# Performance work log

Hardware: AMD Instinct MI355X
Metric: run time of the kernel (lower is better)

The kernel has to match this reference:

```python
import jax, jax.numpy as jnp
import numpy as np

L, B, D, H, P = 4096, 4, 1024, 16, 256
HD = D // H
EPS = 1e-5


def _layer_norm(x, g, b):
    m = jnp.mean(x, axis=-1, keepdims=True)
    v = jnp.mean(jnp.square(x - m), axis=-1, keepdims=True)
    return (x - m) / jnp.sqrt(v + EPS) * g + b


def setup_inputs() -> dict:
    key = jax.random.key(0)
    ks = jax.random.split(key, 8)
    w = lambda k, shape: jax.random.normal(k, shape, jnp.float32) * 0.02
    return {
        "query": jax.random.normal(ks[0], (L, B, D), jnp.float32),
        "q_w": w(ks[1], (D, D)), "q_b": jnp.zeros((D,), jnp.float32),
        "k_w": w(ks[2], (D, D)), "k_b": jnp.zeros((D,), jnp.float32),
        "v_w": w(ks[3], (D, D)), "v_b": jnp.zeros((D,), jnp.float32),
        "e_weight": w(ks[4], (1, H, P, HD)),
        "e_out_w": w(ks[5], (D, D)), "e_out_b": jnp.zeros((D,), jnp.float32),
        "ln_g": jnp.ones((D,), jnp.float32), "ln_b": jnp.zeros((D,), jnp.float32),
        "out_w": w(ks[6], (D, D)), "out_b": jnp.zeros((D,), jnp.float32),
    }


def reference(query, q_w, q_b, k_w, k_b, v_w, v_b, e_weight,
              e_out_w, e_out_b, ln_g, ln_b, out_w, out_b):
    scaling = HD ** -0.5
    # ---- _compute_kv (kv_same=True, no padding mask) ----
    # kv: (L,B,D) -> (B,H,HD,L)
    kvh = query.reshape(L, B, H, HD).transpose(1, 2, 3, 0)
    # pkv = relu(E @ (kv * scaling)) : (B,H,P,L)
    pkv = jax.nn.relu(jnp.einsum('hpd,bhdl->bhpl', e_weight[0], kvh * scaling))
    # kv = pkv @ kv^T : (B,H,P,HD)
    kv = jnp.einsum('bhpl,bhdl->bhpd', pkv, kvh)
    # -> (P,B,D), e_out linear, residual add of e_weight, layer norm
    kv = kv.transpose(2, 0, 1, 3).reshape(P, B, D)
    kv = kv @ e_out_w.T + e_out_b
    kv = kv.reshape(P, B, H, HD) + e_weight.transpose(2, 0, 1, 3)  # broadcast (P,1,H,HD)
    kv = _layer_norm(kv.reshape(P, B, D), ln_g, ln_b)  # (P,B,D)

    # ---- standard MHA against the compressed kv ----
    q = (query @ q_w.T + q_b) * scaling            # (L,B,D)
    k = kv @ k_w.T + k_b                           # (P,B,D)
    v = kv @ v_w.T + v_b                           # (P,B,D)
    qh = q.reshape(L, B, H, HD)
    kh = k.reshape(P, B, H, HD)
    vh = v.reshape(P, B, H, HD)
    logits = jnp.einsum('lbhd,pbhd->bhlp', qh, kh)
    probs = jax.nn.softmax(logits, axis=-1)
    attn = jnp.einsum('bhlp,pbhd->lbhd', probs, vh).reshape(L, B, D)
    return attn @ out_w.T + out_b
```

## Files before the change

### kernel.cpp

```cpp
#include <hip/hip_runtime.h>
#include <hip/hip_bf16.h>
#include <cstdint>
#include <cstddef>

#define LL 4096
#define BB 4
#define DD 1024
#define HH 16
#define PP 256
#define HDD 64
#define LC 16
#define LCHUNK 256

constexpr float kScaling = 0.125f;
constexpr float kEps = 1e-5f;

typedef __attribute__((ext_vector_type(8))) short bf16x8;
typedef __attribute__((ext_vector_type(4))) short short4v;
typedef __attribute__((ext_vector_type(4))) float f32x4;

#define MFMA16(a, b, c) __builtin_amdgcn_mfma_f32_16x16x32_bf16((a), (b), (c), 0, 0, 0)

__device__ __forceinline__ unsigned short f2bf(float f) {
  unsigned int u = __builtin_bit_cast(unsigned int, f);
  u += 0x7FFFu + ((u >> 16) & 1u);
  return (unsigned short)(u >> 16);
}
__device__ __forceinline__ float bf2f(unsigned short u) {
  return __builtin_bit_cast(float, ((unsigned int)u) << 16);
}

__device__ __forceinline__ void gll16(const void* g, void* l) {
  __builtin_amdgcn_global_load_lds(
      (const __attribute__((address_space(1))) unsigned int*)g,
      (__attribute__((address_space(3))) unsigned int*)l, 16, 0, 0);
}

__global__ __launch_bounds__(256) void k_cvt_all(
    const float* __restrict__ q,
    const float* __restrict__ w0, const float* __restrict__ w1,
    const float* __restrict__ w2, const float* __restrict__ w3,
    const float* __restrict__ w4, const float* __restrict__ w5,
    unsigned short* __restrict__ dq,
    unsigned short* __restrict__ d0, unsigned short* __restrict__ d1,
    unsigned short* __restrict__ d2, unsigned short* __restrict__ d3,
    unsigned short* __restrict__ d4, unsigned short* __restrict__ d5) {
  int i = blockIdx.x * 256 + threadIdx.x;
  const float* src; unsigned short* dst; int off;
  if (i < 2097152) { src = q; dst = dq; off = i; }
  else {
    int j = i - 2097152; int w = j >> 17; off = j & 131071;
    if (w == 0) { src = w0; dst = d0; }
    else if (w == 1) { src = w1; dst = d1; }
    else if (w == 2) { src = w2; dst = d2; }
    else if (w == 3) { src = w3; dst = d3; }
    else if (w == 4) { src = w4; dst = d4; }
    else { if (off >= 32768) return; src = w5; dst = d5; }
  }
  const float4* s = (const float4*)(src + (size_t)off * 8);
  float4 a = s[0], b = s[1];
  bf16x8 o;
  o[0] = f2bf(a.x); o[1] = f2bf(a.y); o[2] = f2bf(a.z); o[3] = f2bf(a.w);
  o[4] = f2bf(b.x); o[5] = f2bf(b.y); o[6] = f2bf(b.z); o[7] = f2bf(b.w);
  *(bf16x8*)(dst + (size_t)off * 8) = o;
}

__global__ __launch_bounds__(256) void k_compress_mfma(
    const unsigned short* __restrict__ qbf, const unsigned short* __restrict__ ewbf,
    unsigned short* __restrict__ parts) {
  const int bh = blockIdx.x, lc = blockIdx.y;
  const int b = bh >> 4, h = bh & 15;
  const int tid = threadIdx.x, wv = tid >> 6, lane = tid & 63;
  const int fr = lane & 15, fg = lane >> 4;

  __shared__ __align__(16) char Xl[8192];
  __shared__ __align__(16) char Xtl[8192];
  __shared__ __align__(16) char Pl[32768];

  bf16x8 ef[4][2];
#pragma unroll
  for (int pt = 0; pt < 4; ++pt)
#pragma unroll
    for (int kc = 0; kc < 2; ++kc)
      ef[pt][kc] = *(const bf16x8*)(ewbf +
          (size_t)((h * PP + wv * 64 + pt * 16 + fr) * HDD) + kc * 32 + fg * 8);

  f32x4 acc[4][4];
#pragma unroll
  for (int i = 0; i < 4; ++i)
#pragma unroll
    for (int j = 0; j < 4; ++j) acc[i][j] = (f32x4){0.f, 0.f, 0.f, 0.f};

  const int l0 = lc * LCHUNK;
  for (int t = 0; t < 4; ++t) {
    __syncthreads();
    {
      int l2 = tid >> 3, c8 = tid & 7;
      int l = 2 * l2;
      const unsigned short* xp = qbf +
          ((size_t)(l0 + t * 64 + l) * BB + b) * DD + h * HDD + c8 * 8;
      bf16x8 v0 = *(const bf16x8*)xp;
      bf16x8 v1 = *(const bf16x8*)(xp + BB * DD);
      *(bf16x8*)(Xl + l * 128 + ((c8 ^ (l & 7)) << 4)) = v0;
      *(bf16x8*)(Xl + (l + 1) * 128 + ((c8 ^ ((l + 1) & 7)) << 4)) = v1;
#pragma unroll
      for (int i = 0; i < 8; ++i) {
        int dd = c8 * 8 + i;
        unsigned int packed = (unsigned int)(unsigned short)v0[i] |
                              ((unsigned int)(unsigned short)v1[i] << 16);
        *(unsigned int*)(Xtl + dd * 128 +
            ((((l >> 3) ^ (dd & 7) ^ (dd >> 3)) & 7) << 4) + ((l & 7) << 1)) = packed;
      }
    }
    __syncthreads();
#pragma unroll
    for (int lt = 0; lt < 4; ++lt) {
      int rl = lt * 16 + fr;
      bf16x8 xa0 = *(const bf16x8*)(Xl + rl * 128 + (((0 + fg) ^ (rl & 7)) << 4));
      bf16x8 xa1 = *(const bf16x8*)(Xl + rl * 128 + (((4 + fg) ^ (rl & 7)) << 4));
#pragma unroll
      for (int pt = 0; pt < 4; ++pt) {
        f32x4 s = (f32x4){0.f, 0.f, 0.f, 0.f};
        s = MFMA16(xa0, ef[pt][0], s);
        s = MFMA16(xa1, ef[pt][1], s);
        short4v pk;
#pragma unroll
        for (int r = 0; r < 4; ++r)
          pk[r] = (short)f2bf(fmaxf(s[r] * kScaling, 0.f));
        int p = wv * 64 + pt * 16 + fr;
        int lbase = lt * 16 + fg * 4;
        int slot = lbase >> 3;
        *(short4v*)(Pl + p * 128 + ((slot ^ (p & 7)) << 4) + ((lbase & 7) << 1)) = pk;
      }
    }
    asm volatile("s_waitcnt lgkmcnt(0)" ::: "memory");
    __builtin_amdgcn_sched_barrier(0);
#pragma unroll
    for (int kc = 0; kc < 2; ++kc) {
      bf16x8 pa[4], xb[4];
#pragma unroll
      for (int pt = 0; pt < 4; ++pt) {
        int p = wv * 64 + pt * 16 + fr;
        pa[pt] = *(const bf16x8*)(Pl + p * 128 + (((kc * 4 + fg) ^ (p & 7)) << 4));
      }
#pragma unroll
      for (int dt = 0; dt < 4; ++dt) {
        int dd = dt * 16 + fr;
        xb[dt] = *(const bf16x8*)(Xtl + dd * 128 +
                  ((((kc * 4 + fg) ^ (dd & 7) ^ (dd >> 3)) & 7) << 4));
      }
#pragma unroll
      for (int pt = 0; pt < 4; ++pt)
#pragma unroll
        for (int dt = 0; dt < 4; ++dt)
          acc[pt][dt] = MFMA16(pa[pt], xb[dt], acc[pt][dt]);
    }
  }
  unsigned short* op = parts + (size_t)(lc * 64 + bh) * PP * HDD;
#pragma unroll
  for (int pt = 0; pt < 4; ++pt)
#pragma unroll
    for (int dt = 0; dt < 4; ++dt)
#pragma unroll
      for (int r = 0; r < 4; ++r) {
        int p = wv * 64 + pt * 16 + fg * 4 + r;
        int dd = dt * 16 + fr;
        op[(size_t)p * HDD + dd] = f2bf(acc[pt][dt][r]);
      }
}

__global__ __launch_bounds__(256) void k_reduce(const unsigned short* __restrict__ parts,
                                                unsigned short* __restrict__ kv_raw_bf) {
  int i = blockIdx.x * 256 + threadIdx.x;
  float s = 0.f;
#pragma unroll
  for (int lcc = 0; lcc < LC; ++lcc) s += bf2f(parts[(size_t)lcc * (64 * PP * HDD) + i]);
  int d = i & 63, p = (i >> 6) & 255, bh = i >> 14;
  int b = bh >> 4, h = bh & 15;
  kv_raw_bf[(size_t)(p * BB + b) * DD + h * HDD + d] = f2bf(s);
}

template <int MODE, typename OUTT>
__device__ __forceinline__ void gemm_body(
    const unsigned short* __restrict__ A, const unsigned short* __restrict__ W,
    const float* __restrict__ bias, const float* __restrict__ ew,
    OUTT* __restrict__ C, int m0, int n0, char* Al, char* Bl) {
  const int tid = threadIdx.x;
  const int wv = tid >> 6, lane = tid & 63;
  const int fr = lane & 15, fg = lane >> 4;
  const int wr = wv >> 1, wc = wv & 1;

  f32x4 acc[4][4];
#pragma unroll
  for (int i = 0; i < 4; ++i)
#pragma unroll
    for (int j = 0; j < 4; ++j) acc[i][j] = (f32x4){0.f, 0.f, 0.f, 0.f};

  for (int k0 = 0; k0 < DD; k0 += 64) {
    __syncthreads();
#pragma unroll
    for (int j = 0; j < 4; ++j) {
      int u = tid + j * 256;
      int row = u >> 3, slot = u & 7;
      size_t gcol = (size_t)(k0 + 8 * (slot ^ (row & 7)));
      gll16(A + (size_t)(m0 + row) * DD + gcol, Al + u * 16);
      gll16(W + (size_t)(n0 + row) * DD + gcol, Bl + u * 16);
    }
    __syncthreads();
#pragma unroll
    for (int kc = 0; kc < 2; ++kc) {
      bf16x8 af[4], bfr[4];
#pragma unroll
      for (int mt = 0; mt < 4; ++mt) {
        int r = wr * 64 + mt * 16 + fr;
        af[mt] = *(const bf16x8*)(Al + r * 128 + (((kc * 4 + fg) ^ (r & 7)) << 4));
      }
#pragma unroll
      for (int nt = 0; nt < 4; ++nt) {
        int r = wc * 64 + nt * 16 + fr;
        bfr[nt] = *(const bf16x8*)(Bl + r * 128 + (((kc * 4 + fg) ^ (r & 7)) << 4));
      }
#pragma unroll
      for (int mt = 0; mt < 4; ++mt)
#pragma unroll
        for (int nt = 0; nt < 4; ++nt)
          acc[mt][nt] = MFMA16(af[mt], bfr[nt], acc[mt][nt]);
    }
  }

  float bs[4];
#pragma unroll
  for (int nt = 0; nt < 4; ++nt) bs[nt] = bias[n0 + wc * 64 + nt * 16 + fr];
#pragma unroll
  for (int mt = 0; mt < 4; ++mt)
#pragma unroll
    for (int nt = 0; nt < 4; ++nt) {
      int n = n0 + wc * 64 + nt * 16 + fr;
#pragma unroll
      for (int r = 0; r < 4; ++r) {
        int m = m0 + wr * 64 + mt * 16 + fg * 4 + r;
        float v = acc[mt][nt][r] + bs[nt];
        if (MODE == 1) v *= kScaling;
        if (MODE == 2) {
          int p = m >> 2, hh = n >> 6, d2 = n & 63;
          v += ew[(size_t)((hh << 8) + p) * HDD + d2];
        }
        if constexpr (sizeof(OUTT) == 2)
          C[(size_t)m * DD + n] = (OUTT)f2bf(v);
        else
          C[(size_t)m * DD + n] = v;
      }
    }
}

template <int MODE, typename OUTT>
__global__ __launch_bounds__(256) void k_gemm_mfma(
    const unsigned short* __restrict__ A, const unsigned short* __restrict__ W,
    const float* __restrict__ bias, const float* __restrict__ ew,
    OUTT* __restrict__ C) {
  __shared__ __align__(16) char Al[16384];
  __shared__ __align__(16) char Bl[16384];
  gemm_body<MODE, OUTT>(A, W, bias, ew, C, blockIdx.x * 128, blockIdx.y * 128, Al, Bl);
}

__global__ __launch_bounds__(256) void k_gemm_kv(
    const unsigned short* __restrict__ A,
    const unsigned short* __restrict__ Wk, const unsigned short* __restrict__ Wv,
    const float* __restrict__ kb, const float* __restrict__ vb,
    unsigned short* __restrict__ Ck, unsigned short* __restrict__ Cv) {
  __shared__ __align__(16) char Al[16384];
  __shared__ __align__(16) char Bl[16384];
  if (blockIdx.z == 0)
    gemm_body<0, unsigned short>(A, Wk, kb, nullptr, Ck,
                                 blockIdx.x * 128, blockIdx.y * 128, Al, Bl);
  else
    gemm_body<0, unsigned short>(A, Wv, vb, nullptr, Cv,
                                 blockIdx.x * 128, blockIdx.y * 128, Al, Bl);
}

template <int MODE, typename OUTT>
__global__ __launch_bounds__(512, 2) void k_gemm256(
    const unsigned short* __restrict__ A, const unsigned short* __restrict__ W,
    const float* __restrict__ bias, OUTT* __restrict__ C) {
  __shared__ __align__(16) char lds[131072];
  const int tid = threadIdx.x;
  const int wv = tid >> 6, lane = tid & 63;
  const int fr = lane & 15, fg = lane >> 4;
  const int wm = wv >> 2, wn = wv & 3;
  const int m0 = blockIdx.x * 256, n0 = blockIdx.y * 256;
  const int srow = tid >> 2, sslot = tid & 3;

  auto stageHalf = [&](const unsigned short* __restrict__ G, int g0, int colbase,
                       int dstBase) {
#pragma unroll
    for (int j = 0; j < 2; ++j) {
      int row = srow + j * 128;
      int gs = sslot ^ ((row >> 1) & 3);
      gll16(G + (size_t)(g0 + row) * DD + colbase + gs * 8,
            lds + dstBase + (tid + j * 512) * 16);
    }
  };
  auto rdA = [&](int mf, int kc, int cb) -> bf16x8 {
    int r = wm * 128 + mf * 16 + fr;
    return *(const bf16x8*)(lds + cb + kc * 16384 + r * 64 +
                            ((fg ^ ((r >> 1) & 3)) << 4));
  };
  auto rdB = [&](int nf, int kc, int cb) -> bf16x8 {
    int r = wn * 64 + nf * 16 + fr;
    return *(const bf16x8*)(lds + cb + 32768 + kc * 16384 + r * 64 +
                            ((fg ^ ((r >> 1) & 3)) << 4));
  };

  f32x4 acc[8][4];
#pragma unroll
  for (int i = 0; i < 8; ++i)
#pragma unroll
    for (int j = 0; j < 4; ++j) acc[i][j] = (f32x4){0.f, 0.f, 0.f, 0.f};
  bf16x8 a[8], b[4];

  stageHalf(A, m0, 0, 0);
  stageHalf(W, n0, 0, 32768);
  stageHalf(A, m0, 32, 16384);
  stageHalf(W, n0, 32, 32768 + 16384);
  stageHalf(A, m0, 64, 65536);
  stageHalf(W, n0, 64, 65536 + 32768);
  asm volatile("s_waitcnt vmcnt(4)" ::: "memory");
  __builtin_amdgcn_s_barrier();

  const int NT = DD / 64;
  for (int t = 0; t < NT; ++t) {
    const int cb = (t & 1) << 16;
    const int nb = cb ^ 65536;
    const int k1 = (t + 1) * 64, k2 = (t + 2) * 64;

#pragma unroll
    for (int i = 0; i < 8; ++i) a[i] = rdA(i, 0, cb);
#pragma unroll
    for (int i = 0; i < 4; ++i) b[i] = rdB(i, 0, cb);
    if (t + 1 < NT) {
      stageHalf(A, m0, k1 + 32, nb + 16384);
      stageHalf(W, n0, k1 + 32, nb + 32768 + 16384);
    }
    asm volatile("s_waitcnt lgkmcnt(0)" ::: "memory");
    __builtin_amdgcn_sched_barrier(0);
    __builtin_amdgcn_s_setprio(1);
#pragma unroll
    for (int mf = 0; mf < 8; ++mf)
#pragma unroll
      for (int nf = 0; nf < 4; ++nf)
        acc[mf][nf] = MFMA16(a[mf], b[nf], acc[mf][nf]);
    __builtin_amdgcn_s_setprio(0);
    __builtin_amdgcn_s_barrier();

#pragma unroll
    for (int i = 0; i < 8; ++i) a[i] = rdA(i, 1, cb);
#pragma unroll
    for (int i = 0; i < 4; ++i) b[i] = rdB(i, 1, cb);
    if (t + 2 < NT) {
      stageHalf(A, m0, k2, cb);
      stageHalf(W, n0, k2, cb + 32768);
    }
    asm volatile("s_waitcnt lgkmcnt(0)" ::: "memory");
    __builtin_amdgcn_sched_barrier(0);
    __builtin_amdgcn_s_setprio(1);
#pragma unroll
    for (int mf = 0; mf < 8; ++mf)
#pragma unroll
      for (int nf = 0; nf < 4; ++nf)
        acc[mf][nf] = MFMA16(a[mf], b[nf], acc[mf][nf]);
    __builtin_amdgcn_s_setprio(0);
    if (t + 2 < NT) {
      asm volatile("s_waitcnt vmcnt(4)" ::: "memory");
    } else if (t + 1 < NT) {
      asm volatile("s_waitcnt vmcnt(0)" ::: "memory");
    }
    __builtin_amdgcn_s_barrier();
  }

  float bs[4];
#pragma unroll
  for (int nf = 0; nf < 4; ++nf) bs[nf] = bias[n0 + wn * 64 + nf * 16 + fr];
#pragma unroll
  for (int mf = 0; mf < 8; ++mf)
#pragma unroll
    for (int nf = 0; nf < 4; ++nf) {
      int n = n0 + wn * 64 + nf * 16 + fr;
#pragma unroll
      for (int r = 0; r < 4; ++r) {
        int m = m0 + wm * 128 + mf * 16 + fg * 4 + r;
        float v = acc[mf][nf][r] + bs[nf];
        if (MODE == 1) v *= kScaling;
        if constexpr (sizeof(OUTT) == 2)
          C[(size_t)m * DD + n] = (OUTT)f2bf(v);
        else
          C[(size_t)m * DD + n] = v;
      }
    }
}

__global__ __launch_bounds__(256) void k_ln(const float* __restrict__ x,
                                            const float* __restrict__ g,
                                            const float* __restrict__ bb,
                                            unsigned short* __restrict__ y) {
  const int r = blockIdx.x;
  const int tid = threadIdx.x;
  const float* xr = x + (size_t)r * DD;
  float4 v = *(const float4*)(xr + tid * 4);
  float s1 = v.x + v.y + v.z + v.w;
  float s2 = v.x * v.x + v.y * v.y + v.z * v.z + v.w * v.w;
#pragma unroll
  for (int off = 32; off > 0; off >>= 1) {
    s1 += __shfl_down(s1, off);
    s2 += __shfl_down(s2, off);
  }
  __shared__ float w1[4], w2[4];
  if ((tid & 63) == 0) { w1[tid >> 6] = s1; w2[tid >> 6] = s2; }
  __syncthreads();
  float S1 = w1[0] + w1[1] + w1[2] + w1[3];
  float S2 = w2[0] + w2[1] + w2[2] + w2[3];
  float mean = S1 * (1.f / DD);
  float var = S2 * (1.f / DD) - mean * mean;
  float rstd = rsqrtf(var + kEps);
  float4 gv = *(const float4*)(g + tid * 4);
  float4 bv = *(const float4*)(bb + tid * 4);
  short4v o;
  o[0] = (short)f2bf((v.x - mean) * rstd * gv.x + bv.x);
  o[1] = (short)f2bf((v.y - mean) * rstd * gv.y + bv.y);
  o[2] = (short)f2bf((v.z - mean) * rstd * gv.z + bv.z);
  o[3] = (short)f2bf((v.w - mean) * rstd * gv.w + bv.w);
  *(short4v*)(y + (size_t)r * DD + tid * 4) = o;
}

__global__ __launch_bounds__(512, 2) void k_attn_mfma(
    const unsigned short* __restrict__ qbf, const unsigned short* __restrict__ kbf,
    const unsigned short* __restrict__ vbf, unsigned short* __restrict__ attn) {
  const int bh = blockIdx.y;
  const int b = bh >> 4, h = bh & 15;
  const int tid = threadIdx.x, wv = tid >> 6, lane = tid & 63;
  const int fr = lane & 15, fg = lane >> 4;
  const int bl0 = blockIdx.x * 128;

  __shared__ __align__(16) char Kl[16384];
  __shared__ __align__(16) char Vt[16384];
  __shared__ __align__(16) char Pl[32768];

  const size_t qrow = ((size_t)(bl0 + wv * 16 + fr) * BB + b) * DD + h * HDD;
  bf16x8 qf0 = *(const bf16x8*)(qbf + qrow + fg * 8);
  bf16x8 qf1 = *(const bf16x8*)(qbf + qrow + 32 + fg * 8);

  f32x4 o[4];
#pragma unroll
  for (int dt = 0; dt < 4; ++dt) o[dt] = (f32x4){0.f, 0.f, 0.f, 0.f};
  float psum = 0.f;
  char* Pw = Pl + wv * 4096;

  for (int ph = 0; ph < 2; ++ph) {
    __syncthreads();
#pragma unroll
    for (int j = 0; j < 2; ++j) {
      int u = tid + j * 512;
      int p = u >> 3, slot = u & 7;
      gll16(kbf + ((size_t)((ph * 128 + p) * BB + b)) * DD + h * HDD +
                8 * (slot ^ (p & 7)),
            Kl + u * 16);
    }
    {
      int p2 = tid >> 3, c8 = tid & 7;
      int p0 = ph * 128 + 2 * p2;
      const unsigned short* vp = vbf + ((size_t)(p0 * BB + b)) * DD + h * HDD + c8 * 8;
      bf16x8 v0 = *(const bf16x8*)vp;
      bf16x8 v1 = *(const bf16x8*)(vp + BB * DD);
      int pl = (2 * p2) & 63, pc = p2 >> 5;
      char* base = Vt + pc * 8192;
#pragma unroll
      for (int i = 0; i < 8; ++i) {
        int dd = c8 * 8 + i;
        unsigned int packed = (unsigned int)(unsigned short)v0[i] |
                              ((unsigned int)(unsigned short)v1[i] << 16);
        *(unsigned int*)(base + dd * 128 +
            ((((pl >> 3) ^ (dd & 7) ^ (dd >> 3)) & 7) << 4) + ((pl & 7) << 1)) = packed;
      }
    }
    __syncthreads();

    f32x4 s[8];
    __builtin_amdgcn_s_setprio(1);
#pragma unroll
    for (int pt = 0; pt < 8; ++pt) {
      int pr = pt * 16 + fr;
      bf16x8 a0 = *(const bf16x8*)(Kl + pr * 128 + ((fg ^ (pr & 7)) << 4));
      bf16x8 a1 = *(const bf16x8*)(Kl + pr * 128 + (((4 + fg) ^ (pr & 7)) << 4));
      f32x4 acc = (f32x4){0.f, 0.f, 0.f, 0.f};
      acc = MFMA16(a0, qf0, acc);
      acc = MFMA16(a1, qf1, acc);
      s[pt] = acc;
    }
    __builtin_amdgcn_s_setprio(0);

#pragma unroll
    for (int pt = 0; pt < 8; ++pt) {
      float e0 = __expf(s[pt][0]), e1 = __expf(s[pt][1]);
      float e2 = __expf(s[pt][2]), e3 = __expf(s[pt][3]);
      psum += (e0 + e1) + (e2 + e3);
      short4v pk;
      pk[0] = (short)f2bf(e0); pk[1] = (short)f2bf(e1);
      pk[2] = (short)f2bf(e2); pk[3] = (short)f2bf(e3);
      int pbyte = (pt * 16 + fg * 4) * 2;
      int slot = pbyte >> 4, rem = pbyte & 15;
      *(short4v*)(Pw + fr * 256 + ((slot ^ (fr & 7)) << 4) + rem) = pk;
    }
    asm volatile("s_waitcnt lgkmcnt(0)" ::: "memory");
    __builtin_amdgcn_sched_barrier(0);

    __builtin_amdgcn_s_setprio(1);
#pragma unroll
    for (int kc = 0; kc < 4; ++kc) {
      int slot = kc * 4 + fg;
      bf16x8 pa = *(const bf16x8*)(Pw + fr * 256 + ((slot ^ (fr & 7)) << 4));
      int sl2 = (kc & 1) * 4 + fg;
#pragma unroll
      for (int dt = 0; dt < 4; ++dt) {
        int dd = dt * 16 + fr;
        bf16x8 vb = *(const bf16x8*)(Vt + (kc >> 1) * 8192 + dd * 128 +
                     (((sl2 ^ (dd & 7) ^ (dd >> 3)) & 7) << 4));
        o[dt] = MFMA16(pa, vb, o[dt]);
      }
    }
    __builtin_amdgcn_s_setprio(0);
  }

  psum += __shfl_xor(psum, 16);
  psum += __shfl_xor(psum, 32);

#pragma unroll
  for (int r = 0; r < 4; ++r) {
    int lloc = fg * 4 + r;
    float inv = 1.f / __shfl(psum, lloc);
    unsigned short* op = attn +
        ((size_t)(bl0 + wv * 16 + lloc) * BB + b) * DD + h * HDD;
#pragma unroll
    for (int dt = 0; dt < 4; ++dt)
      op[dt * 16 + fr] = f2bf(o[dt][r] * inv);
  }
}

extern "C" void kernel_launch(void* const* d_in, const int* in_sizes, int n_in,
                              void* d_out, int out_size, void* d_ws, size_t ws_size,
                              hipStream_t stream) {
  const float* query   = (const float*)d_in[0];
  const float* q_w     = (const float*)d_in[1];
  const float* q_b     = (const float*)d_in[2];
  const float* k_w     = (const float*)d_in[3];
  const float* k_b     = (const float*)d_in[4];
  const float* v_w     = (const float*)d_in[5];
  const float* v_b     = (const float*)d_in[6];
  const float* e_weight= (const float*)d_in[7];
  const float* e_out_w = (const float*)d_in[8];
  const float* e_out_b = (const float*)d_in[9];
  const float* ln_g    = (const float*)d_in[10];
  const float* ln_b    = (const float*)d_in[11];
  const float* out_w   = (const float*)d_in[12];
  const float* out_b   = (const float*)d_in[13];
  float* out = (float*)d_out;

  char* w = (char*)d_ws;
  unsigned short* parts   = (unsigned short*)w;
  unsigned short* q_bf    = (unsigned short*)w;
  unsigned short* attn_bf = (unsigned short*)(w + (32u << 20));
  unsigned short* query_bf= (unsigned short*)(w + (64u << 20));
  unsigned short* kv_raw  = (unsigned short*)(w + (96u << 20));
  float* kv_eo            = (float*)(w + (98u << 20));
  unsigned short* kv_ln   = (unsigned short*)(w + (102u << 20));
  unsigned short* k_buf   = (unsigned short*)(w + (104u << 20));
  unsigned short* v_buf   = (unsigned short*)(w + (106u << 20));
  unsigned short* wq  = (unsigned short*)(w + (108u << 20));
  unsigned short* wk  = (unsigned short*)(w + (110u << 20));
  unsigned short* wv_ = (unsigned short*)(w + (112u << 20));
  unsigned short* weo = (unsigned short*)(w + (114u << 20));
  unsigned short* wo  = (unsigned short*)(w + (116u << 20));
  unsigned short* ewb = (unsigned short*)(w + (118u << 20));

  k_cvt_all<<<10880, 256, 0, stream>>>(query, q_w, k_w, v_w, e_out_w, out_w, e_weight,
                                       query_bf, wq, wk, wv_, weo, wo, ewb);

  k_compress_mfma<<<dim3(64, LC), 256, 0, stream>>>(query_bf, ewb, parts);
  k_reduce<<<4096, 256, 0, stream>>>(parts, kv_raw);
  k_gemm_mfma<2, float><<<dim3(8, 8), 256, 0, stream>>>(kv_raw, weo, e_out_b, e_weight, kv_eo);
  k_ln<<<PP * BB, 256, 0, stream>>>(kv_eo, ln_g, ln_b, kv_ln);
  k_gemm256<1, unsigned short><<<dim3(64, 4), 512, 0, stream>>>(query_bf, wq, q_b, q_bf);
  k_gemm_kv<<<dim3(8, 8, 2), 256, 0, stream>>>(kv_ln, wk, wv_, k_b, v_b, k_buf, v_buf);
  k_attn_mfma<<<dim3(32, 64), 512, 0, stream>>>(q_bf, k_buf, v_buf, attn_bf);
  k_gemm256<0, float><<<dim3(64, 4), 512, 0, stream>>>(attn_bf, wo, out_b, out);
}
```

Before: 213.0 us.

## Fuse query bf16 conversion into compress kernel and vectorize partial reduction

```diff
diff --git a/kernel.cpp b/kernel.cpp
--- a/kernel.cpp
+++ b/kernel.cpp
@@ -36,27 +36,22 @@
       (__attribute__((address_space(3))) unsigned int*)l, 16, 0, 0);
 }
 
-__global__ __launch_bounds__(256) void k_cvt_all(
-    const float* __restrict__ q,
+__global__ __launch_bounds__(256) void k_cvt_w(
     const float* __restrict__ w0, const float* __restrict__ w1,
     const float* __restrict__ w2, const float* __restrict__ w3,
     const float* __restrict__ w4, const float* __restrict__ w5,
-    unsigned short* __restrict__ dq,
     unsigned short* __restrict__ d0, unsigned short* __restrict__ d1,
     unsigned short* __restrict__ d2, unsigned short* __restrict__ d3,
     unsigned short* __restrict__ d4, unsigned short* __restrict__ d5) {
   int i = blockIdx.x * 256 + threadIdx.x;
-  const float* src; unsigned short* dst; int off;
-  if (i < 2097152) { src = q; dst = dq; off = i; }
-  else {
-    int j = i - 2097152; int w = j >> 17; off = j & 131071;
-    if (w == 0) { src = w0; dst = d0; }
-    else if (w == 1) { src = w1; dst = d1; }
-    else if (w == 2) { src = w2; dst = d2; }
-    else if (w == 3) { src = w3; dst = d3; }
-    else if (w == 4) { src = w4; dst = d4; }
-    else { if (off >= 32768) return; src = w5; dst = d5; }
-  }
+  int w = i >> 17, off = i & 131071;
+  const float* src; unsigned short* dst;
+  if (w == 0) { src = w0; dst = d0; }
+  else if (w == 1) { src = w1; dst = d1; }
+  else if (w == 2) { src = w2; dst = d2; }
+  else if (w == 3) { src = w3; dst = d3; }
+  else if (w == 4) { src = w4; dst = d4; }
+  else { if (off >= 32768) return; src = w5; dst = d5; }
   const float4* s = (const float4*)(src + (size_t)off * 8);
   float4 a = s[0], b = s[1];
   bf16x8 o;
@@ -66,8 +61,8 @@
 }
 
 __global__ __launch_bounds__(256) void k_compress_mfma(
-    const unsigned short* __restrict__ qbf, const unsigned short* __restrict__ ewbf,
-    unsigned short* __restrict__ parts) {
+    const float* __restrict__ q32, const unsigned short* __restrict__ ewbf,
+    unsigned short* __restrict__ qbf_out, unsigned short* __restrict__ parts) {
   const int bh = blockIdx.x, lc = blockIdx.y;
   const int b = bh >> 4, h = bh & 15;
   const int tid = threadIdx.x, wv = tid >> 6, lane = tid & 63;
@@ -97,10 +92,19 @@
     {
       int l2 = tid >> 3, c8 = tid & 7;
       int l = 2 * l2;
-      const unsigned short* xp = qbf +
-          ((size_t)(l0 + t * 64 + l) * BB + b) * DD + h * HDD + c8 * 8;
-      bf16x8 v0 = *(const bf16x8*)xp;
-      bf16x8 v1 = *(const bf16x8*)(xp + BB * DD);
+      size_t rowbase = ((size_t)(l0 + t * 64 + l) * BB + b) * DD + h * HDD + c8 * 8;
+      const float* xp = q32 + rowbase;
+      float4 a0 = *(const float4*)xp;
+      float4 a1 = *(const float4*)(xp + 4);
+      float4 b0 = *(const float4*)(xp + BB * DD);
+      float4 b1 = *(const float4*)(xp + BB * DD + 4);
+      bf16x8 v0, v1;
+      v0[0] = f2bf(a0.x); v0[1] = f2bf(a0.y); v0[2] = f2bf(a0.z); v0[3] = f2bf(a0.w);
+      v0[4] = f2bf(a1.x); v0[5] = f2bf(a1.y); v0[6] = f2bf(a1.z); v0[7] = f2bf(a1.w);
+      v1[0] = f2bf(b0.x); v1[1] = f2bf(b0.y); v1[2] = f2bf(b0.z); v1[3] = f2bf(b0.w);
+      v1[4] = f2bf(b1.x); v1[5] = f2bf(b1.y); v1[6] = f2bf(b1.z); v1[7] = f2bf(b1.w);
+      *(bf16x8*)(qbf_out + rowbase) = v0;
+      *(bf16x8*)(qbf_out + rowbase + BB * DD) = v1;
       *(bf16x8*)(Xl + l * 128 + ((c8 ^ (l & 7)) << 4)) = v0;
       *(bf16x8*)(Xl + (l + 1) * 128 + ((c8 ^ ((l + 1) & 7)) << 4)) = v1;
 #pragma unroll
@@ -171,13 +175,22 @@
 
 __global__ __launch_bounds__(256) void k_reduce(const unsigned short* __restrict__ parts,
                                                 unsigned short* __restrict__ kv_raw_bf) {
-  int i = blockIdx.x * 256 + threadIdx.x;
-  float s = 0.f;
-#pragma unroll
-  for (int lcc = 0; lcc < LC; ++lcc) s += bf2f(parts[(size_t)lcc * (64 * PP * HDD) + i]);
+  int u = blockIdx.x * 256 + threadIdx.x;
+  size_t off = (size_t)u * 8;
+  float s[8] = {0.f, 0.f, 0.f, 0.f, 0.f, 0.f, 0.f, 0.f};
+#pragma unroll
+  for (int lcc = 0; lcc < LC; ++lcc) {
+    bf16x8 v = *(const bf16x8*)(parts + (size_t)lcc * (64 * PP * HDD) + off);
+#pragma unroll
+    for (int j = 0; j < 8; ++j) s[j] += bf2f((unsigned short)v[j]);
+  }
+  int i = (int)off;
   int d = i & 63, p = (i >> 6) & 255, bh = i >> 14;
   int b = bh >> 4, h = bh & 15;
-  kv_raw_bf[(size_t)(p * BB + b) * DD + h * HDD + d] = f2bf(s);
+  bf16x8 o;
+#pragma unroll
+  for (int j = 0; j < 8; ++j) o[j] = (short)f2bf(s[j]);
+  *(bf16x8*)(kv_raw_bf + (size_t)(p * BB + b) * DD + h * HDD + d) = o;
 }
 
 template <int MODE, typename OUTT>
@@ -580,11 +593,11 @@
   unsigned short* wo  = (unsigned short*)(w + (116u << 20));
   unsigned short* ewb = (unsigned short*)(w + (118u << 20));
 
-  k_cvt_all<<<10880, 256, 0, stream>>>(query, q_w, k_w, v_w, e_out_w, out_w, e_weight,
-                                       query_bf, wq, wk, wv_, weo, wo, ewb);
-
-  k_compress_mfma<<<dim3(64, LC), 256, 0, stream>>>(query_bf, ewb, parts);
-  k_reduce<<<4096, 256, 0, stream>>>(parts, kv_raw);
+  k_cvt_w<<<2688, 256, 0, stream>>>(q_w, k_w, v_w, e_out_w, out_w, e_weight,
+                                    wq, wk, wv_, weo, wo, ewb);
+
+  k_compress_mfma<<<dim3(64, LC), 256, 0, stream>>>(query, ewb, query_bf, parts);
+  k_reduce<<<512, 256, 0, stream>>>(parts, kv_raw);
   k_gemm_mfma<2, float><<<dim3(8, 8), 256, 0, stream>>>(kv_raw, weo, e_out_b, e_weight, kv_eo);
   k_ln<<<PP * BB, 256, 0, stream>>>(kv_eo, ln_g, ln_b, kv_ln);
   k_gemm256<1, unsigned short><<<dim3(64, 4), 512, 0, stream>>>(query_bf, wq, q_b, q_bf);
```

Measured after the change: 209.8 us. No clear change (-1.5%).
